# Performance work log

Measured on AMD Instinct MI355X. Metric: run time of the kernel, lower is better.

## Reference

```python
import jax, jax.numpy as jnp
import numpy as np

ALPHA = 0.2  # LeakyReLU negative slope
NEG = -9e15


def setup_inputs() -> dict:
    key = jax.random.key(0)
    k1, k2, k3, k4 = jax.random.split(key, 4)
    N, F_in, F_out = 8192, 512, 64
    h = jax.random.normal(k1, (N, F_in), dtype=jnp.float32)
    adj = jax.random.randint(k2, (N, N), 0, 2, dtype=jnp.int32)
    # xavier_uniform with gain=1.414
    def xavier(k, shape, gain=1.414):
        fan_in, fan_out = shape[0], shape[1]
        bound = gain * np.sqrt(6.0 / (fan_in + fan_out))
        return jax.random.uniform(k, shape, jnp.float32, -bound, bound)
    W = xavier(k3, (F_in, F_out))
    a = xavier(k4, (2 * F_out, 1))
    return {"h": h, "adj": adj, "W": W, "a": a}


def reference(h, adj, W, a):
    F_out = W.shape[1]
    Wh = h @ W                                   # [N, F_out]
    # e_ij = LeakyReLU([Wh_i || Wh_j] . a) = LeakyReLU(Wh.a1 + (Wh.a2)^T)
    e1 = Wh @ a[:F_out, 0]                       # [N]
    e2 = Wh @ a[F_out:, 0]                       # [N]
    e = jax.nn.leaky_relu(e1[:, None] + e2[None, :], ALPHA)  # [N, N]
    e = jnp.where(adj > 0, e, NEG)
    attention = jax.nn.softmax(e, axis=1)        # dropout p=0.0 -> identity
    h_prime = attention @ Wh                     # [N, F_out]
    return jax.nn.elu(h_prime)                   # concat=True
```

## Files before the change

kernel.cpp:

```cpp
#include <hip/hip_runtime.h>
#include <hip/hip_bf16.h>
#include <stdint.h>

typedef __attribute__((ext_vector_type(8))) short short8;
typedef __attribute__((ext_vector_type(4))) float f32x4;

#define NSLICE 8
#define SLICE_J 1024
#define CHUNKS 16
#define L2E 1.44269504f
#define L2E5 0.288539008f

static __device__ __forceinline__ short f2bf(float f) {
    unsigned int u = __float_as_uint(f);
    u += 0x7fffu + ((u >> 16) & 1u);
    return (short)(u >> 16);
}

static __device__ __forceinline__ int pk2(float a, float b) {
    float2 f2 = make_float2(a, b);
    __hip_bfloat162 h = __float22bfloat162_rn(f2);
    return *reinterpret_cast<int*>(&h);
}

__global__ __launch_bounds__(256)
void gat_wh(const float* __restrict__ h, const float* __restrict__ W,
            const float* __restrict__ a, short* __restrict__ whT,
            float* __restrict__ e1, float* __restrict__ e2)
{
    const int lane = threadIdx.x & 63;
    const int wave = threadIdx.x >> 6;
    const int row0 = blockIdx.x * 8 + wave * 2;

    float acc[2] = {0.f, 0.f};
#pragma unroll 8
    for (int c = 0; c < 512; ++c) {
        const float wv = W[c * 64 + lane];
#pragma unroll
        for (int r = 0; r < 2; ++r)
            acc[r] += h[(size_t)(row0 + r) * 512 + c] * wv;
    }

    const float a1v = a[lane];
    const float a2v = a[64 + lane];
    const int f    = lane >> 4;
    const int r16n = lane & 15;
#pragma unroll
    for (int r = 0; r < 2; ++r) {
        float p1 = acc[r] * a1v;
        float p2 = acc[r] * a2v;
#pragma unroll
        for (int off = 32; off; off >>= 1) {
            p1 += __shfl_xor(p1, off);
            p2 += __shfl_xor(p2, off);
        }
        if (lane == 0) { e1[row0 + r] = p1; e2[row0 + r] = p2; }
        const int j = row0 + r;
        const int kin = j & 63;
        const int frag = (kin >> 5) & 1, qk = (kin >> 3) & 3, t = kin & 7;
        whT[(size_t)(j >> 6) * 4096 + (f * 2 + frag) * 512 + qk * 128 + r16n * 8 + t]
            = f2bf(acc[r]);
    }
}

__global__ __launch_bounds__(256)
void gat_attn(const int* __restrict__ adj, const short* __restrict__ whT,
              const float* __restrict__ e1, const float* __restrict__ e2,
              float* __restrict__ lpart, float* __restrict__ opart)
{
    __shared__ __align__(16) float2 sB[SLICE_J];
    const int bid = blockIdx.x;
    const int s   = bid & (NSLICE - 1);
    const int rb  = bid >> 3;
    const int tid = threadIdx.x;

    {
        const float4 v = *reinterpret_cast<const float4*>(e2 + s * SLICE_J + tid * 4);
        float4 lo, hi;
        lo.x = __builtin_amdgcn_exp2f(v.x * L2E);  lo.y = __builtin_amdgcn_exp2f(v.x * L2E5);
        lo.z = __builtin_amdgcn_exp2f(v.y * L2E);  lo.w = __builtin_amdgcn_exp2f(v.y * L2E5);
        hi.x = __builtin_amdgcn_exp2f(v.z * L2E);  hi.y = __builtin_amdgcn_exp2f(v.z * L2E5);
        hi.z = __builtin_amdgcn_exp2f(v.w * L2E);  hi.w = __builtin_amdgcn_exp2f(v.w * L2E5);
        reinterpret_cast<float4*>(sB)[tid * 2]     = lo;
        reinterpret_cast<float4*>(sB)[tid * 2 + 1] = hi;
    }
    __syncthreads();

    const int lane = tid & 63;
    const int wave = tid >> 6;
    const int quad = lane >> 4;
    const int r16  = lane & 15;
    const int rowBase = rb * 64 + wave * 16;
    const int row  = rowBase + r16;
    const float e1v = e1[row];
    const float a1 = __builtin_amdgcn_exp2f(e1v * L2E);
    const float a5 = __builtin_amdgcn_exp2f(e1v * L2E5);
    const size_t adjRow = (size_t)row * 8192 + (size_t)s * SLICE_J;

    float ls0 = 0.f, ls1 = 0.f, ls2 = 0.f, ls3 = 0.f;
    f32x4 acc[4];
#pragma unroll
    for (int ff = 0; ff < 4; ++ff) acc[ff] = (f32x4){0.f, 0.f, 0.f, 0.f};

    const int jq = quad * 8;
    int4 A0 = *reinterpret_cast<const int4*>(adj + adjRow + jq);
    int4 A1 = *reinterpret_cast<const int4*>(adj + adjRow + jq + 4);
    int4 A2 = *reinterpret_cast<const int4*>(adj + adjRow + jq + 32);
    int4 A3 = *reinterpret_cast<const int4*>(adj + adjRow + jq + 36);

    for (int ch = 0; ch < CHUNKS; ++ch) {
        const int chn = (ch + 1) & (CHUNKS - 1);
        const size_t nbase = adjRow + chn * 64 + jq;
        const int4 N0 = *reinterpret_cast<const int4*>(adj + nbase);
        const int4 N1 = *reinterpret_cast<const int4*>(adj + nbase + 4);
        const int4 N2 = *reinterpret_cast<const int4*>(adj + nbase + 32);
        const int4 N3 = *reinterpret_cast<const int4*>(adj + nbase + 36);

        const int j0 = ch * 64 + jq;
        const float4 P0 = *reinterpret_cast<const float4*>(&sB[j0]);
        const float4 P1 = *reinterpret_cast<const float4*>(&sB[j0 + 2]);
        const float4 P2 = *reinterpret_cast<const float4*>(&sB[j0 + 4]);
        const float4 P3 = *reinterpret_cast<const float4*>(&sB[j0 + 6]);
        const float4 P4 = *reinterpret_cast<const float4*>(&sB[j0 + 32]);
        const float4 P5 = *reinterpret_cast<const float4*>(&sB[j0 + 34]);
        const float4 P6 = *reinterpret_cast<const float4*>(&sB[j0 + 36]);
        const float4 P7 = *reinterpret_cast<const float4*>(&sB[j0 + 38]);

        float w0  = (A0.x > 0) ? fmaxf(a1 * P0.x, a5 * P0.y) : 0.f;
        float w1  = (A0.y > 0) ? fmaxf(a1 * P0.z, a5 * P0.w) : 0.f;
        float w2  = (A0.z > 0) ? fmaxf(a1 * P1.x, a5 * P1.y) : 0.f;
        float w3  = (A0.w > 0) ? fmaxf(a1 * P1.z, a5 * P1.w) : 0.f;
        float w4  = (A1.x > 0) ? fmaxf(a1 * P2.x, a5 * P2.y) : 0.f;
        float w5  = (A1.y > 0) ? fmaxf(a1 * P2.z, a5 * P2.w) : 0.f;
        float w6  = (A1.z > 0) ? fmaxf(a1 * P3.x, a5 * P3.y) : 0.f;
        float w7  = (A1.w > 0) ? fmaxf(a1 * P3.z, a5 * P3.w) : 0.f;
        float w8  = (A2.x > 0) ? fmaxf(a1 * P4.x, a5 * P4.y) : 0.f;
        float w9  = (A2.y > 0) ? fmaxf(a1 * P4.z, a5 * P4.w) : 0.f;
        float w10 = (A2.z > 0) ? fmaxf(a1 * P5.x, a5 * P5.y) : 0.f;
        float w11 = (A2.w > 0) ? fmaxf(a1 * P5.z, a5 * P5.w) : 0.f;
        float w12 = (A3.x > 0) ? fmaxf(a1 * P6.x, a5 * P6.y) : 0.f;
        float w13 = (A3.y > 0) ? fmaxf(a1 * P6.z, a5 * P6.w) : 0.f;
        float w14 = (A3.z > 0) ? fmaxf(a1 * P7.x, a5 * P7.y) : 0.f;
        float w15 = (A3.w > 0) ? fmaxf(a1 * P7.z, a5 * P7.w) : 0.f;

        ls0 += w0 + w1 + w2 + w3;
        ls1 += w4 + w5 + w6 + w7;
        ls2 += w8 + w9 + w10 + w11;
        ls3 += w12 + w13 + w14 + w15;

        union { int4 i; short8 s; } U0, U1;
        U0.i = make_int4(pk2(w0, w1),  pk2(w2, w3),  pk2(w4, w5),  pk2(w6, w7));
        U1.i = make_int4(pk2(w8, w9),  pk2(w10, w11), pk2(w12, w13), pk2(w14, w15));

        const short* wtile = whT + (size_t)(s * 16 + ch) * 4096 + lane * 8;
#pragma unroll
        for (int ff = 0; ff < 4; ++ff) {
            const short8 b0 = *reinterpret_cast<const short8*>(wtile + (ff * 2 + 0) * 512);
            const short8 b1 = *reinterpret_cast<const short8*>(wtile + (ff * 2 + 1) * 512);
            acc[ff] = __builtin_amdgcn_mfma_f32_16x16x32_bf16(U0.s, b0, acc[ff], 0, 0, 0);
            acc[ff] = __builtin_amdgcn_mfma_f32_16x16x32_bf16(U1.s, b1, acc[ff], 0, 0, 0);
        }

        A0 = N0; A1 = N1; A2 = N2; A3 = N3;
    }

    float lsum = (ls0 + ls1) + (ls2 + ls3);
    lsum += __shfl_xor(lsum, 16);
    lsum += __shfl_xor(lsum, 32);
    if (lane < 16) lpart[s * 8192 + rowBase + lane] = lsum;

#pragma unroll
    for (int ff = 0; ff < 4; ++ff) {
#pragma unroll
        for (int rg = 0; rg < 4; ++rg) {
            const int orow = rowBase + quad * 4 + rg;
            const int ocol = ff * 16 + r16;
            opart[((size_t)s * 8192 + orow) * 64 + ocol] = acc[ff][rg];
        }
    }
}

__global__ __launch_bounds__(256)
void gat_combine(const float* __restrict__ lpart, const float* __restrict__ opart,
                 float* __restrict__ out)
{
    const int gid = blockIdx.x * 256 + threadIdx.x;
    const int row = gid >> 6;
    const int f   = gid & 63;

    float lsum = 0.f, osum = 0.f;
#pragma unroll
    for (int s = 0; s < NSLICE; ++s) {
        lsum += lpart[s * 8192 + row];
        osum += opart[((size_t)s * 8192 + row) * 64 + f];
    }
    const float v = osum / lsum;
    out[gid] = (v > 0.f) ? v : (__expf(v) - 1.f);
}

extern "C" void kernel_launch(void* const* d_in, const int* in_sizes, int n_in,
                              void* d_out, int out_size, void* d_ws, size_t ws_size,
                              hipStream_t stream) {
    const float* h   = (const float*)d_in[0];
    const int*   adj = (const int*)d_in[1];
    const float* W   = (const float*)d_in[2];
    const float* a   = (const float*)d_in[3];
    float* out = (float*)d_out;

    char* ws = (char*)d_ws;
    short* whT   = (short*)ws;
    float* e1    = (float*)(ws + (1u << 20));
    float* e2    = (float*)(ws + (1u << 20) + (32u << 10));
    float* lpart = (float*)(ws + (1u << 20) + (64u << 10));
    float* opart = (float*)(ws + (2u << 20));

    gat_wh<<<1024, 256, 0, stream>>>(h, W, a, whT, e1, e2);
    gat_attn<<<128 * NSLICE, 256, 0, stream>>>(adj, whT, e1, e2, lpart, opart);
    gat_combine<<<out_size / 256, 256, 0, stream>>>(lpart, opart, out);
}
```

Measured before the change: 453.3 us.

## Pack adjacency into a bitmask in a pre-pass before attention

Adds a streaming kernel that compresses the int32 adjacency matrix into one bit per entry, stored in workspace. The attention kernel then reads 8 bytes of mask per chunk instead of sixteen int4 loads of adjacency, which removes the wide, latency-heavy global loads from its inner loop. This is meant to make the attention kernel lighter and less stalled on memory. In exchange, the full adjacency is still read once by the new pass, and the change adds a kernel launch, a mask write and more workspace use.

```diff
diff --git a/kernel.cpp b/kernel.cpp
--- a/kernel.cpp
+++ b/kernel.cpp
@@ -21,6 +21,24 @@
     float2 f2 = make_float2(a, b);
     __hip_bfloat162 h = __float22bfloat162_rn(f2);
     return *reinterpret_cast<int*>(&h);
+}
+
+__global__ __launch_bounds__(256)
+void gat_pack(const int* __restrict__ adj, unsigned char* __restrict__ bm)
+{
+    const int g = blockIdx.x * 256 + threadIdx.x;
+    const int4 a0 = reinterpret_cast<const int4*>(adj)[(size_t)g * 2];
+    const int4 a1 = reinterpret_cast<const int4*>(adj)[(size_t)g * 2 + 1];
+    unsigned int m = 0;
+    m |= (a0.x > 0) ? 1u   : 0u;
+    m |= (a0.y > 0) ? 2u   : 0u;
+    m |= (a0.z > 0) ? 4u   : 0u;
+    m |= (a0.w > 0) ? 8u   : 0u;
+    m |= (a1.x > 0) ? 16u  : 0u;
+    m |= (a1.y > 0) ? 32u  : 0u;
+    m |= (a1.z > 0) ? 64u  : 0u;
+    m |= (a1.w > 0) ? 128u : 0u;
+    bm[g] = (unsigned char)m;
 }
 
 __global__ __launch_bounds__(256)
@@ -64,7 +82,7 @@
 }
 
 __global__ __launch_bounds__(256)
-void gat_attn(const int* __restrict__ adj, const short* __restrict__ whT,
+void gat_attn(const unsigned char* __restrict__ bm, const short* __restrict__ whT,
               const float* __restrict__ e1, const float* __restrict__ e2,
               float* __restrict__ lpart, float* __restrict__ opart)
 {
@@ -95,28 +113,20 @@
     const float e1v = e1[row];
     const float a1 = __builtin_amdgcn_exp2f(e1v * L2E);
     const float a5 = __builtin_amdgcn_exp2f(e1v * L2E5);
-    const size_t adjRow = (size_t)row * 8192 + (size_t)s * SLICE_J;
+    const unsigned char* bmRow = bm + (size_t)row * 1024 + s * 128;
+    const int qs = quad * 8;
 
     float ls0 = 0.f, ls1 = 0.f, ls2 = 0.f, ls3 = 0.f;
     f32x4 acc[4];
 #pragma unroll
     for (int ff = 0; ff < 4; ++ff) acc[ff] = (f32x4){0.f, 0.f, 0.f, 0.f};
 
-    const int jq = quad * 8;
-    int4 A0 = *reinterpret_cast<const int4*>(adj + adjRow + jq);
-    int4 A1 = *reinterpret_cast<const int4*>(adj + adjRow + jq + 4);
-    int4 A2 = *reinterpret_cast<const int4*>(adj + adjRow + jq + 32);
-    int4 A3 = *reinterpret_cast<const int4*>(adj + adjRow + jq + 36);
-
     for (int ch = 0; ch < CHUNKS; ++ch) {
-        const int chn = (ch + 1) & (CHUNKS - 1);
-        const size_t nbase = adjRow + chn * 64 + jq;
-        const int4 N0 = *reinterpret_cast<const int4*>(adj + nbase);
-        const int4 N1 = *reinterpret_cast<const int4*>(adj + nbase + 4);
-        const int4 N2 = *reinterpret_cast<const int4*>(adj + nbase + 32);
-        const int4 N3 = *reinterpret_cast<const int4*>(adj + nbase + 36);
-
-        const int j0 = ch * 64 + jq;
+        const uint2 M = *reinterpret_cast<const uint2*>(bmRow + ch * 8);
+        const unsigned int lo = M.x >> qs;
+        const unsigned int hi = M.y >> qs;
+
+        const int j0 = ch * 64 + qs;
         const float4 P0 = *reinterpret_cast<const float4*>(&sB[j0]);
         const float4 P1 = *reinterpret_cast<const float4*>(&sB[j0 + 2]);
         const float4 P2 = *reinterpret_cast<const float4*>(&sB[j0 + 4]);
@@ -126,22 +136,22 @@
         const float4 P6 = *reinterpret_cast<const float4*>(&sB[j0 + 36]);
         const float4 P7 = *reinterpret_cast<const float4*>(&sB[j0 + 38]);
 
-        float w0  = (A0.x > 0) ? fmaxf(a1 * P0.x, a5 * P0.y) : 0.f;
-        float w1  = (A0.y > 0) ? fmaxf(a1 * P0.z, a5 * P0.w) : 0.f;
-        float w2  = (A0.z > 0) ? fmaxf(a1 * P1.x, a5 * P1.y) : 0.f;
-        float w3  = (A0.w > 0) ? fmaxf(a1 * P1.z, a5 * P1.w) : 0.f;
-        float w4  = (A1.x > 0) ? fmaxf(a1 * P2.x, a5 * P2.y) : 0.f;
-        float w5  = (A1.y > 0) ? fmaxf(a1 * P2.z, a5 * P2.w) : 0.f;
-        float w6  = (A1.z > 0) ? fmaxf(a1 * P3.x, a5 * P3.y) : 0.f;
-        float w7  = (A1.w > 0) ? fmaxf(a1 * P3.z, a5 * P3.w) : 0.f;
-        float w8  = (A2.x > 0) ? fmaxf(a1 * P4.x, a5 * P4.y) : 0.f;
-        float w9  = (A2.y > 0) ? fmaxf(a1 * P4.z, a5 * P4.w) : 0.f;
-        float w10 = (A2.z > 0) ? fmaxf(a1 * P5.x, a5 * P5.y) : 0.f;
-        float w11 = (A2.w > 0) ? fmaxf(a1 * P5.z, a5 * P5.w) : 0.f;
-        float w12 = (A3.x > 0) ? fmaxf(a1 * P6.x, a5 * P6.y) : 0.f;
-        float w13 = (A3.y > 0) ? fmaxf(a1 * P6.z, a5 * P6.w) : 0.f;
-        float w14 = (A3.z > 0) ? fmaxf(a1 * P7.x, a5 * P7.y) : 0.f;
-        float w15 = (A3.w > 0) ? fmaxf(a1 * P7.z, a5 * P7.w) : 0.f;
+        float w0  = (lo & 1u)   ? fmaxf(a1 * P0.x, a5 * P0.y) : 0.f;
+        float w1  = (lo & 2u)   ? fmaxf(a1 * P0.z, a5 * P0.w) : 0.f;
+        float w2  = (lo & 4u)   ? fmaxf(a1 * P1.x, a5 * P1.y) : 0.f;
+        float w3  = (lo & 8u)   ? fmaxf(a1 * P1.z, a5 * P1.w) : 0.f;
+        float w4  = (lo & 16u)  ? fmaxf(a1 * P2.x, a5 * P2.y) : 0.f;
+        float w5  = (lo & 32u)  ? fmaxf(a1 * P2.z, a5 * P2.w) : 0.f;
+        float w6  = (lo & 64u)  ? fmaxf(a1 * P3.x, a5 * P3.y) : 0.f;
+        float w7  = (lo & 128u) ? fmaxf(a1 * P3.z, a5 * P3.w) : 0.f;
+        float w8  = (hi & 1u)   ? fmaxf(a1 * P4.x, a5 * P4.y) : 0.f;
+        float w9  = (hi & 2u)   ? fmaxf(a1 * P4.z, a5 * P4.w) : 0.f;
+        float w10 = (hi & 4u)   ? fmaxf(a1 * P5.x, a5 * P5.y) : 0.f;
+        float w11 = (hi & 8u)   ? fmaxf(a1 * P5.z, a5 * P5.w) : 0.f;
+        float w12 = (hi & 16u)  ? fmaxf(a1 * P6.x, a5 * P6.y) : 0.f;
+        float w13 = (hi & 32u)  ? fmaxf(a1 * P6.z, a5 * P6.w) : 0.f;
+        float w14 = (hi & 64u)  ? fmaxf(a1 * P7.x, a5 * P7.y) : 0.f;
+        float w15 = (hi & 128u) ? fmaxf(a1 * P7.z, a5 * P7.w) : 0.f;
 
         ls0 += w0 + w1 + w2 + w3;
         ls1 += w4 + w5 + w6 + w7;
@@ -149,7 +159,7 @@
         ls3 += w12 + w13 + w14 + w15;
 
         union { int4 i; short8 s; } U0, U1;
-        U0.i = make_int4(pk2(w0, w1),  pk2(w2, w3),  pk2(w4, w5),  pk2(w6, w7));
+        U0.i = make_int4(pk2(w0, w1),  pk2(w2, w3),   pk2(w4, w5),   pk2(w6, w7));
         U1.i = make_int4(pk2(w8, w9),  pk2(w10, w11), pk2(w12, w13), pk2(w14, w15));
 
         const short* wtile = whT + (size_t)(s * 16 + ch) * 4096 + lane * 8;
@@ -160,8 +170,6 @@
             acc[ff] = __builtin_amdgcn_mfma_f32_16x16x32_bf16(U0.s, b0, acc[ff], 0, 0, 0);
             acc[ff] = __builtin_amdgcn_mfma_f32_16x16x32_bf16(U1.s, b1, acc[ff], 0, 0, 0);
         }
-
-        A0 = N0; A1 = N1; A2 = N2; A3 = N3;
     }
 
     float lsum = (ls0 + ls1) + (ls2 + ls3);
@@ -213,8 +221,10 @@
     float* e2    = (float*)(ws + (1u << 20) + (32u << 10));
     float* lpart = (float*)(ws + (1u << 20) + (64u << 10));
     float* opart = (float*)(ws + (2u << 20));
-
+    unsigned char* bmask = (unsigned char*)(ws + (32u << 20));
+
+    gat_pack<<<32768, 256, 0, stream>>>(adj, bmask);
     gat_wh<<<1024, 256, 0, stream>>>(h, W, a, whT, e1, e2);
-    gat_attn<<<128 * NSLICE, 256, 0, stream>>>(adj, whT, e1, e2, lpart, opart);
+    gat_attn<<<128 * NSLICE, 256, 0, stream>>>(bmask, whT, e1, e2, lpart, opart);
     gat_combine<<<out_size / 256, 256, 0, stream>>>(lpart, opart, out);
 }
```

After: 449.4 us. Within noise of the previous version (-0.9%).
